# Kernel tuning notes

Measured on AMD Instinct MI355X. Metric: run time of the kernel, lower is better.

## Reference

```python
import jax, jax.numpy as jnp
import numpy as np
from functools import partial

B, T, F = 4096, 256, 32
H1, H2, NT = 64, 32, 3


def _lstm_layer(x, W_ih, W_hh, b_ih, b_hh):
    """Torch-style LSTM (batch_first). x: [B,T,Fin], W_ih: [4H,Fin], W_hh: [4H,H].
    Gate order i, f, g, o. Returns all hidden states [B,T,H]."""
    Bsz = x.shape[0]
    H = W_hh.shape[1]
    # Precompute input contribution for all timesteps (one big GEMM)
    xg = jnp.einsum('btf,gf->btg', x, W_ih) + b_ih + b_hh  # [B,T,4H]

    def step(carry, xg_t):
        h, c = carry
        gates = xg_t + h @ W_hh.T  # [B,4H]
        i, f, g, o = jnp.split(gates, 4, axis=-1)
        i = jax.nn.sigmoid(i)
        f = jax.nn.sigmoid(f)
        g = jnp.tanh(g)
        o = jax.nn.sigmoid(o)
        c = f * c + i * g
        h = o * jnp.tanh(c)
        return (h, c), h

    init = (jnp.zeros((Bsz, H), x.dtype), jnp.zeros((Bsz, H), x.dtype))
    _, hs = jax.lax.scan(step, init, jnp.swapaxes(xg, 0, 1))  # hs: [T,B,H]
    return jnp.swapaxes(hs, 0, 1)


def setup_inputs() -> dict:
    key = jax.random.key(0)
    ks = jax.random.split(key, 12)
    s1 = 1.0 / np.sqrt(H1)
    s2 = 1.0 / np.sqrt(H2)
    u = lambda k, shape, s: jax.random.uniform(k, shape, jnp.float32, -s, s)
    return {
        'x': jax.random.normal(ks[0], (B, T, F), jnp.float32),
        'W_ih1': u(ks[1], (4 * H1, F), s1),
        'W_hh1': u(ks[2], (4 * H1, H1), s1),
        'b_ih1': u(ks[3], (4 * H1,), s1),
        'b_hh1': u(ks[4], (4 * H1,), s1),
        'W_ih2': u(ks[5], (4 * H2, H1), s2),
        'W_hh2': u(ks[6], (4 * H2, H2), s2),
        'b_ih2': u(ks[7], (4 * H2,), s2),
        'b_hh2': u(ks[8], (4 * H2,), s2),
        'W_head': u(ks[9], (NT, H2), s2),
        'b_head': u(ks[10], (NT,), s2),
    }


def reference(x, W_ih1, W_hh1, b_ih1, b_hh1, W_ih2, W_hh2, b_ih2, b_hh2, W_head, b_head):
    h1 = _lstm_layer(x, W_ih1, W_hh1, b_ih1, b_hh1)   # [B,T,64]; dropout is identity in eval
    h2 = _lstm_layer(h1, W_ih2, W_hh2, b_ih2, b_hh2)  # [B,T,32]
    last = h2[:, -1, :]                               # [B,32]
    return last @ W_head.T + b_head                   # [B,3]
```

## Files before the change

### kernel.cpp

```cpp
#include <hip/hip_runtime.h>

#define Bsz 4096
#define Tt  256
#define Ff  32
#define H1  64
#define H2  32
#define NTAPS 3
#define BT  8
#define NTHR 512
#define CH  16

typedef _Float16 half8  __attribute__((ext_vector_type(8)));
typedef __fp16   fp16x2 __attribute__((ext_vector_type(2)));
typedef float    f32x4  __attribute__((ext_vector_type(4)));

#define H1S 72
#define H2S 40
#define HDS 33

__device__ __forceinline__ float lstm_unit(float pi, float pf, float pg, float po,
                                           float& c) {
    const float K1 = 1.4426950408889634f;
    float ei = __builtin_amdgcn_exp2f(-K1 * pi);
    float ef = __builtin_amdgcn_exp2f(-K1 * pf);
    float eg = __builtin_amdgcn_exp2f(-2.0f * K1 * __builtin_fabsf(pg));
    float eo = __builtin_amdgcn_exp2f(-K1 * po);
    float p1 = (1.0f + ei) * (1.0f + eg);
    float pf1 = 1.0f + ef;
    float R  = __builtin_amdgcn_rcpf(p1 * pf1);
    float t1 = c * p1;
    float t2 = __builtin_copysignf(1.0f - eg, pg) * pf1;
    c = (t1 + t2) * R;
    float ec = __builtin_amdgcn_exp2f(-2.0f * K1 * __builtin_fabsf(c));
    float th = (1.0f - ec) * __builtin_amdgcn_rcpf((1.0f + eo) * (1.0f + ec));
    return __builtin_copysignf(th, c);
}

#define MFMA16(a, b, c) __builtin_amdgcn_mfma_f32_16x16x32_f16((a), (b), (c), 0, 0, 0)

__device__ __forceinline__ void dma16(const float* gp, const float* lp) {
    __builtin_amdgcn_global_load_lds(
        (const __attribute__((address_space(1))) void*)gp,
        (__attribute__((address_space(3))) void*)lp, 16, 0, 0);
}

__device__ __forceinline__ half8 cvt8(f32x4 lo, f32x4 hi) {
    union { half8 v; fp16x2 h[4]; } ax;
    ax.h[0] = __builtin_amdgcn_cvt_pkrtz(lo[0], lo[1]);
    ax.h[1] = __builtin_amdgcn_cvt_pkrtz(lo[2], lo[3]);
    ax.h[2] = __builtin_amdgcn_cvt_pkrtz(hi[0], hi[1]);
    ax.h[3] = __builtin_amdgcn_cvt_pkrtz(hi[2], hi[3]);
    return ax.v;
}

__global__ __launch_bounds__(NTHR, 4)
void lstm2_fused(const float* __restrict__ x,
                 const float* __restrict__ Wih1, const float* __restrict__ Whh1,
                 const float* __restrict__ bih1, const float* __restrict__ bhh1,
                 const float* __restrict__ Wih2, const float* __restrict__ Whh2,
                 const float* __restrict__ bih2, const float* __restrict__ bhh2,
                 const float* __restrict__ Whead, const float* __restrict__ bhead,
                 float* __restrict__ out)
{
    __shared__ __align__(16) _Float16 sH1[2][BT][H1S];
    __shared__ __align__(16) _Float16 sH2[2][BT][H2S];
    __shared__ __align__(16) float    sXC[2][CH][8][BT][4];
    __shared__ __align__(16) float    sXG[2][4][4][64][4];
    __shared__ __align__(16) float    sHead[BT][HDS];

    const int tid  = threadIdx.x;
    const int wid  = tid >> 6;
    const int lane = tid & 63;
    const int l15  = lane & 15;
    const int q    = lane >> 4;
    const int row8 = l15 & 7;
    const int b0   = blockIdx.x * BT;
    const int u    = wid & 3;
    const bool isL1 = (wid < 4);

    const int colL1 = u * 16 + l15;
    const int r0  = (q >> 1) * 2, r1v = r0 + 1;
    const int bLo = (q & 1) * 4 + (q >> 1) * 2;
    const int hT = u & 1, rh = u >> 1;
    const int rL2 = (q >> 1) * 2 + rh;
    const int bL2 = (q & 1) * 4 + (q >> 1) * 2 + rh;

    const int bL  = lane & 7;
    const int f4L = lane >> 3;
    const float* gbase = x + (size_t)(b0 + bL) * Tt * Ff + f4L * 4;

    if (!isL1) {
        #pragma unroll
        for (int j = 0; j < 4; ++j) {
            int tl = u * 4 + j;
            dma16(gbase + (size_t)tl * Ff, &sXC[0][tl][0][0][0]);
        }
    }

    half8 wL[4][3];
    half8 wX[4];
    float biasA[4], biasX[4];
    if (isL1) {
        #pragma unroll
        for (int G = 0; G < 4; ++G) {
            int gr = G * 64 + colL1;
            #pragma unroll
            for (int c = 0; c < 2; ++c) {
                half8 v;
                #pragma unroll
                for (int e = 0; e < 8; ++e)
                    v[e] = (_Float16)Whh1[gr * H1 + c * 32 + q * 8 + e];
                wL[G][c] = v;
            }
            wL[G][2] = wL[G][1];
            biasA[G] = 0.0f;
            biasX[G] = 0.0f;
        }
    } else {
        #pragma unroll
        for (int G = 0; G < 4; ++G) {
            int gr2 = G * 32 + hT * 16 + l15;
            half8 v0, v1, v2, vx;
            #pragma unroll
            for (int e = 0; e < 8; ++e) {
                int k = q * 8 + e;
                v0[e] = (_Float16)Whh2[gr2 * H2 + k];
                v1[e] = (_Float16)Wih2[gr2 * H1 + k];
                v2[e] = (_Float16)Wih2[gr2 * H1 + 32 + k];
            }
            wL[G][0] = v0; wL[G][1] = v1; wL[G][2] = v2;
            biasA[G] = bih2[gr2] + bhh2[gr2];

            int grx = G * 64 + u * 16 + l15;
            #pragma unroll
            for (int e = 0; e < 8; ++e)
                vx[e] = (_Float16)Wih1[grx * Ff + q * 8 + e];
            wX[G] = vx;
            biasX[G] = bih1[grx] + bhh1[grx];
        }
    }

    for (int idx = tid; idx < BT * H1S; idx += NTHR) ((_Float16*)sH1[1])[idx] = (_Float16)0.0f;
    for (int idx = tid; idx < BT * H2S; idx += NTHR) ((_Float16*)sH2[1])[idx] = (_Float16)0.0f;

    __syncthreads();

    if (!isL1) {
        f32x4 lo = *(const f32x4*)&sXC[0][0][2 * q][row8][0];
        f32x4 hi = *(const f32x4*)&sXC[0][0][2 * q + 1][row8][0];
        half8 ax = cvt8(lo, hi);
        #pragma unroll
        for (int G = 0; G < 4; ++G) {
            f32x4 a = {biasX[G], biasX[G], biasX[G], biasX[G]};
            a = MFMA16(ax, wX[G], a);
            *(f32x4*)&sXG[0][u][G][lane][0] = a;
        }
    }
    __syncthreads();

    float cs0 = 0.0f, cs1 = 0.0f;

    #pragma unroll 2
    for (int i = 0; i < Tt; ++i) {
        const int cur = i & 1, nxt = cur ^ 1;
        const int cbuf = (i >> 4) & 1;

        if (!isL1 && (i & (CH - 1)) == 0 && i + CH < Tt) {
            const float* gb = gbase + (size_t)(i + CH) * Ff;
            #pragma unroll
            for (int j = 0; j < 4; ++j) {
                int tl = u * 4 + j;
                dma16(gb + (size_t)tl * Ff, &sXC[cbuf ^ 1][tl][0][0][0]);
            }
        }

        half8 a0 = *(const half8*)&sH1[nxt][row8][q * 8];
        half8 a1 = *(const half8*)&sH1[nxt][row8][32 + q * 8];

        if (isL1) {
            f32x4 acc[4];
            #pragma unroll
            for (int G = 0; G < 4; ++G) {
                f32x4 a = *(const f32x4*)&sXG[cur][u][G][lane][0];
                a = MFMA16(a0, wL[G][0], a);
                a = MFMA16(a1, wL[G][1], a);
                acc[G] = a;
            }
            float h0  = lstm_unit(acc[0][r0],  acc[1][r0],  acc[2][r0],  acc[3][r0],  cs0);
            float h1v = lstm_unit(acc[0][r1v], acc[1][r1v], acc[2][r1v], acc[3][r1v], cs1);
            sH1[cur][bLo][colL1]     = (_Float16)h0;
            sH1[cur][bLo + 1][colL1] = (_Float16)h1v;
        } else {
            if (i >= 1) {
                half8 ah = *(const half8*)&sH2[cur][row8][q * 8];
                f32x4 acc[4];
                #pragma unroll
                for (int G = 0; G < 4; ++G) {
                    f32x4 a = {biasA[G], biasA[G], biasA[G], biasA[G]};
                    a = MFMA16(ah, wL[G][0], a);
                    a = MFMA16(a0, wL[G][1], a);
                    a = MFMA16(a1, wL[G][2], a);
                    acc[G] = a;
                }
                float hA = lstm_unit(acc[0][rL2], acc[1][rL2], acc[2][rL2], acc[3][rL2], cs0);
                sH2[nxt][bL2][hT * 16 + l15] = (_Float16)hA;
            }
            if (i + 1 < Tt) {
                const int t = i + 1, cb = (t >> 4) & 1, t16 = t & (CH - 1);
                f32x4 lo = *(const f32x4*)&sXC[cb][t16][2 * q][row8][0];
                f32x4 hi = *(const f32x4*)&sXC[cb][t16][2 * q + 1][row8][0];
                half8 ax = cvt8(lo, hi);
                #pragma unroll
                for (int G = 0; G < 4; ++G) {
                    f32x4 a = {biasX[G], biasX[G], biasX[G], biasX[G]};
                    a = MFMA16(ax, wX[G], a);
                    *(f32x4*)&sXG[nxt][u][G][lane][0] = a;
                }
            }
        }

        __syncthreads();
    }

    {
        const int cur = Tt & 1;
        const int nxt = cur ^ 1;
        if (!isL1) {
            half8 a0 = *(const half8*)&sH1[nxt][row8][q * 8];
            half8 a1 = *(const half8*)&sH1[nxt][row8][32 + q * 8];
            half8 ah = *(const half8*)&sH2[cur][row8][q * 8];
            f32x4 acc[4];
            #pragma unroll
            for (int G = 0; G < 4; ++G) {
                f32x4 a = {biasA[G], biasA[G], biasA[G], biasA[G]};
                a = MFMA16(ah, wL[G][0], a);
                a = MFMA16(a0, wL[G][1], a);
                a = MFMA16(a1, wL[G][2], a);
                acc[G] = a;
            }
            float hA = lstm_unit(acc[0][rL2], acc[1][rL2], acc[2][rL2], acc[3][rL2], cs0);
            sHead[bL2][hT * 16 + l15] = hA;
        }
        __syncthreads();
    }

    if (tid < BT * NTAPS) {
        int b = tid / NTAPS, n = tid - b * NTAPS;
        float s = bhead[n];
        #pragma unroll
        for (int k = 0; k < H2; ++k) s = fmaf(sHead[b][k], Whead[n * H2 + k], s);
        out[(size_t)(b0 + b) * NTAPS + n] = s;
    }
}

extern "C" void kernel_launch(void* const* d_in, const int* in_sizes, int n_in,
                              void* d_out, int out_size, void* d_ws, size_t ws_size,
                              hipStream_t stream) {
    const float* xp    = (const float*)d_in[0];
    const float* Wih1  = (const float*)d_in[1];
    const float* Whh1  = (const float*)d_in[2];
    const float* bih1  = (const float*)d_in[3];
    const float* bhh1  = (const float*)d_in[4];
    const float* Wih2  = (const float*)d_in[5];
    const float* Whh2  = (const float*)d_in[6];
    const float* bih2  = (const float*)d_in[7];
    const float* bhh2  = (const float*)d_in[8];
    const float* Whead = (const float*)d_in[9];
    const float* bhead = (const float*)d_in[10];
    float* outp = (float*)d_out;

    hipLaunchKernelGGL(lstm2_fused, dim3(Bsz / BT), dim3(NTHR), 0, stream,
                       xp, Wih1, Whh1, bih1, bhh1, Wih2, Whh2, bih2, bhh2,
                       Whead, bhead, outp);
}
```

Baseline: 471.6 us.

## Move layer-1 input projection into layer-1 warps and keep it in registers

The layer-1 input projection (x·W_ih1 + bias) moves from the layer-2 warps, which staged it through an LDS buffer, into the layer-1 warps themselves. The next step's projection is held in registers (xgN), which removes the sXG shared buffer and its per-step store and load. This balances the per-step MFMA count between the two warp groups, so the layer-2 warps no longer do 16 MFMAs per step while the layer-1 warps do 8. Launch bounds are relaxed from 4 to 2 blocks per CU, giving more register room in exchange for a lower occupancy cap.

Measured after the change: 383.0 us. 1.23x faster.

```diff
diff --git a/kernel.cpp b/kernel.cpp
--- a/kernel.cpp
+++ b/kernel.cpp
@@ -53,7 +53,7 @@
     return ax.v;
 }
 
-__global__ __launch_bounds__(NTHR, 4)
+__global__ __launch_bounds__(NTHR, 2)
 void lstm2_fused(const float* __restrict__ x,
                  const float* __restrict__ Wih1, const float* __restrict__ Whh1,
                  const float* __restrict__ bih1, const float* __restrict__ bhh1,
@@ -65,7 +65,6 @@
     __shared__ __align__(16) _Float16 sH1[2][BT][H1S];
     __shared__ __align__(16) _Float16 sH2[2][BT][H2S];
     __shared__ __align__(16) float    sXC[2][CH][8][BT][4];
-    __shared__ __align__(16) float    sXG[2][4][4][64][4];
     __shared__ __align__(16) float    sHead[BT][HDS];
 
     const int tid  = threadIdx.x;
@@ -97,9 +96,8 @@
         }
     }
 
-    half8 wL[4][3];
-    half8 wX[4];
-    float biasA[4], biasX[4];
+    half8 wH[4][3];
+    float bias[4];
     if (isL1) {
         #pragma unroll
         for (int G = 0; G < 4; ++G) {
@@ -110,17 +108,20 @@
                 #pragma unroll
                 for (int e = 0; e < 8; ++e)
                     v[e] = (_Float16)Whh1[gr * H1 + c * 32 + q * 8 + e];
-                wL[G][c] = v;
-            }
-            wL[G][2] = wL[G][1];
-            biasA[G] = 0.0f;
-            biasX[G] = 0.0f;
+                wH[G][c] = v;
+            }
+            half8 vx;
+            #pragma unroll
+            for (int e = 0; e < 8; ++e)
+                vx[e] = (_Float16)Wih1[gr * Ff + q * 8 + e];
+            wH[G][2] = vx;
+            bias[G] = bih1[gr] + bhh1[gr];
         }
     } else {
         #pragma unroll
         for (int G = 0; G < 4; ++G) {
             int gr2 = G * 32 + hT * 16 + l15;
-            half8 v0, v1, v2, vx;
+            half8 v0, v1, v2;
             #pragma unroll
             for (int e = 0; e < 8; ++e) {
                 int k = q * 8 + e;
@@ -128,15 +129,8 @@
                 v1[e] = (_Float16)Wih2[gr2 * H1 + k];
                 v2[e] = (_Float16)Wih2[gr2 * H1 + 32 + k];
             }
-            wL[G][0] = v0; wL[G][1] = v1; wL[G][2] = v2;
-            biasA[G] = bih2[gr2] + bhh2[gr2];
-
-            int grx = G * 64 + u * 16 + l15;
-            #pragma unroll
-            for (int e = 0; e < 8; ++e)
-                vx[e] = (_Float16)Wih1[grx * Ff + q * 8 + e];
-            wX[G] = vx;
-            biasX[G] = bih1[grx] + bhh1[grx];
+            wH[G][0] = v0; wH[G][1] = v1; wH[G][2] = v2;
+            bias[G] = bih2[gr2] + bhh2[gr2];
         }
     }
 
@@ -145,18 +139,17 @@
 
     __syncthreads();
 
-    if (!isL1) {
+    f32x4 xgN[4];
+    if (isL1) {
         f32x4 lo = *(const f32x4*)&sXC[0][0][2 * q][row8][0];
         f32x4 hi = *(const f32x4*)&sXC[0][0][2 * q + 1][row8][0];
         half8 ax = cvt8(lo, hi);
         #pragma unroll
         for (int G = 0; G < 4; ++G) {
-            f32x4 a = {biasX[G], biasX[G], biasX[G], biasX[G]};
-            a = MFMA16(ax, wX[G], a);
-            *(f32x4*)&sXG[0][u][G][lane][0] = a;
-        }
-    }
-    __syncthreads();
+            f32x4 a = {bias[G], bias[G], bias[G], bias[G]};
+            xgN[G] = MFMA16(ax, wH[G][2], a);
+        }
+    }
 
     float cs0 = 0.0f, cs1 = 0.0f;
 
@@ -181,30 +174,16 @@
             f32x4 acc[4];
             #pragma unroll
             for (int G = 0; G < 4; ++G) {
-                f32x4 a = *(const f32x4*)&sXG[cur][u][G][lane][0];
-                a = MFMA16(a0, wL[G][0], a);
-                a = MFMA16(a1, wL[G][1], a);
+                f32x4 a = xgN[G];
+                a = MFMA16(a0, wH[G][0], a);
+                a = MFMA16(a1, wH[G][1], a);
                 acc[G] = a;
             }
             float h0  = lstm_unit(acc[0][r0],  acc[1][r0],  acc[2][r0],  acc[3][r0],  cs0);
             float h1v = lstm_unit(acc[0][r1v], acc[1][r1v], acc[2][r1v], acc[3][r1v], cs1);
             sH1[cur][bLo][colL1]     = (_Float16)h0;
             sH1[cur][bLo + 1][colL1] = (_Float16)h1v;
-        } else {
-            if (i >= 1) {
-                half8 ah = *(const half8*)&sH2[cur][row8][q * 8];
-                f32x4 acc[4];
-                #pragma unroll
-                for (int G = 0; G < 4; ++G) {
-                    f32x4 a = {biasA[G], biasA[G], biasA[G], biasA[G]};
-                    a = MFMA16(ah, wL[G][0], a);
-                    a = MFMA16(a0, wL[G][1], a);
-                    a = MFMA16(a1, wL[G][2], a);
-                    acc[G] = a;
-                }
-                float hA = lstm_unit(acc[0][rL2], acc[1][rL2], acc[2][rL2], acc[3][rL2], cs0);
-                sH2[nxt][bL2][hT * 16 + l15] = (_Float16)hA;
-            }
+
             if (i + 1 < Tt) {
                 const int t = i + 1, cb = (t >> 4) & 1, t16 = t & (CH - 1);
                 f32x4 lo = *(const f32x4*)&sXC[cb][t16][2 * q][row8][0];
@@ -212,11 +191,23 @@
                 half8 ax = cvt8(lo, hi);
                 #pragma unroll
                 for (int G = 0; G < 4; ++G) {
-                    f32x4 a = {biasX[G], biasX[G], biasX[G], biasX[G]};
-                    a = MFMA16(ax, wX[G], a);
-                    *(f32x4*)&sXG[nxt][u][G][lane][0] = a;
+                    f32x4 a = {bias[G], bias[G], bias[G], bias[G]};
+                    xgN[G] = MFMA16(ax, wH[G][2], a);
                 }
             }
+        } else if (i >= 1) {
+            half8 ah = *(const half8*)&sH2[cur][row8][q * 8];
+            f32x4 acc[4];
+            #pragma unroll
+            for (int G = 0; G < 4; ++G) {
+                f32x4 a = {bias[G], bias[G], bias[G], bias[G]};
+                a = MFMA16(ah, wH[G][0], a);
+                a = MFMA16(a0, wH[G][1], a);
+                a = MFMA16(a1, wH[G][2], a);
+                acc[G] = a;
+            }
+            float hA = lstm_unit(acc[0][rL2], acc[1][rL2], acc[2][rL2], acc[3][rL2], cs0);
+            sH2[nxt][bL2][hT * 16 + l15] = (_Float16)hA;
         }
 
         __syncthreads();
@@ -232,10 +223,10 @@
             f32x4 acc[4];
             #pragma unroll
             for (int G = 0; G < 4; ++G) {
-                f32x4 a = {biasA[G], biasA[G], biasA[G], biasA[G]};
-                a = MFMA16(ah, wL[G][0], a);
-                a = MFMA16(a0, wL[G][1], a);
-                a = MFMA16(a1, wL[G][2], a);
+                f32x4 a = {bias[G], bias[G], bias[G], bias[G]};
+                a = MFMA16(ah, wH[G][0], a);
+                a = MFMA16(a0, wH[G][1], a);
+                a = MFMA16(a1, wH[G][2], a);
                 acc[G] = a;
             }
             float hA = lstm_unit(acc[0][rL2], acc[1][rL2], acc[2][rL2], acc[3][rL2], cs0);
```
